# Kernel tuning notes

Hardware: AMD Instinct MI355X
Metric: run time of the kernel (lower is better)

Reference implementation:

```python
import math
import jax, jax.numpy as jnp
import numpy as np

RATIO = 0.1

def setup_inputs() -> dict:
    key = jax.random.key(0)
    ks = jax.random.split(key, 8)
    B, S, D = 8, 4096, 2048
    transformer_out = jax.random.normal(ks[0], (B, S, D), jnp.float32)
    hidden_states = jax.random.normal(ks[1], (B, S, D), jnp.float32)
    lengths = jax.random.randint(ks[2], (B,), S // 2, S + 1)
    attention_mask = (jnp.arange(S)[None, :] < lengths[:, None]).astype(jnp.int32)
    s = 1.0 / math.sqrt(D)
    W1 = jax.random.normal(ks[3], (D, D), jnp.float32) * s
    b1 = jnp.zeros((D,), jnp.float32)
    w2 = jax.random.normal(ks[4], (D,), jnp.float32) * s
    b2 = jnp.zeros((), jnp.float32)
    Wv = jax.random.normal(ks[5], (D, D), jnp.float32) * s
    bv = jnp.zeros((D,), jnp.float32)
    return dict(transformer_out=transformer_out, hidden_states=hidden_states,
                attention_mask=attention_mask, W1=W1, b1=b1, w2=w2, b2=b2, Wv=Wv, bv=bv)

def reference(transformer_out, hidden_states, attention_mask, W1, b1, w2, b2, Wv, bv):
    B, S, D = transformer_out.shape
    M = math.ceil(S * RATIO)  # static upper bound on max_nugget (n_nugget <= ceil(S*ratio))
    # scorer MLP: Linear(D,D) -> ReLU -> Linear(D,1), squeezed
    h = jax.nn.relu(jnp.einsum('bsd,de->bse', transformer_out, W1) + b1)
    scores = jnp.einsum('bse,e->bs', h, w2) + b2                      # [B,S]
    maskb = attention_mask.astype(bool)
    scores = jnp.where(maskb, scores, jnp.finfo(scores.dtype).min)    # masked fill
    n_token = maskb.sum(axis=1)                                        # [B]
    n_nugget = jnp.ceil(n_token.astype(scores.dtype) * RATIO).astype(jnp.int32)
    n_nugget = jnp.minimum(jnp.maximum(n_nugget, 1), n_token)
    nugget_mask = jnp.arange(M)[None, :] < n_nugget[:, None]          # [B,M] ragged validity
    # descending top-k by double argsort, then stable reorder to original token order
    sorted_idx = jnp.argsort(-scores, axis=1)[:, :M]                   # [B,M]
    big = jnp.iinfo(sorted_idx.dtype).max
    resort = jnp.where(nugget_mask, sorted_idx, big)
    indices = jnp.take_along_axis(sorted_idx, jnp.argsort(resort, axis=1), axis=1)
    enc = jnp.take_along_axis(hidden_states, indices[:, :, None], axis=1)  # [B,M,D]
    enc = jnp.einsum('bmd,de->bme', enc, Wv) + bv                      # value_ffn
    nugget_scores = jnp.take_along_axis(scores, indices, axis=1)       # [B,M]
    return enc, nugget_mask, nugget_scores, indices, scores
```

## Files before the change

### kernel.cpp

```cpp
#include <hip/hip_runtime.h>
#include <float.h>
#include <math.h>

typedef _Float16 h16;
typedef _Float16 h16x8 __attribute__((ext_vector_type(8)));
typedef float    f32x4 __attribute__((ext_vector_type(4)));

#define MFMA16(a, b, c) __builtin_amdgcn_mfma_f32_16x16x32_f16((a), (b), (c), 0, 0, 0)

#define B_    8
#define S_    4096
#define D_    2048
#define M_    410
#define MROWS (B_ * S_)
#define R2    (B_ * M_)

#define MASK_FILL (-3.3895313892515355e38f)

#define ENC_OFF  0
#define MASK_OFF (B_ * M_ * D_)
#define NSC_OFF  (MASK_OFF + B_ * M_)
#define IDX_OFF  (NSC_OFF + B_ * M_)
#define SC_OFF   (IDX_OFF + B_ * M_)

#define WS_W1T  ((size_t)0)
#define WS_WVT  ((size_t)8  << 20)
#define WS_PART ((size_t)16 << 20)
#define WS_IDX  ((size_t)17 << 20)
#define WS_NEEDED (((size_t)17 << 20) + R2 * sizeof(int))

__device__ inline float finite_or(float v, float alt) {
    return (v == v && v <= FLT_MAX && v >= -FLT_MAX) ? v : alt;
}

__device__ inline void gload_lds16(const h16* g, h16* l) {
    __builtin_amdgcn_global_load_lds(
        (const __attribute__((address_space(1))) void*)g,
        (__attribute__((address_space(3))) void*)l, 16, 0, 0);
}

__device__ inline h16x8 cvt8(f32x4 a, f32x4 b) {
    h16x8 r;
#pragma unroll
    for (int i = 0; i < 4; ++i) { r[i] = (h16)a[i]; r[i + 4] = (h16)b[i]; }
    return r;
}

__global__ __launch_bounds__(256) void transpose_kernel(
    const float* __restrict__ W1, const float* __restrict__ Wv,
    h16* __restrict__ w1t, h16* __restrict__ wvt)
{
    __shared__ float tile[32][33];
    const float* src = blockIdx.z ? Wv : W1;
    h16* dt = blockIdx.z ? wvt : w1t;
    const int tx = threadIdx.x, ty = threadIdx.y;
    const int n0 = blockIdx.x * 32, k0 = blockIdx.y * 32;
#pragma unroll
    for (int i = 0; i < 4; ++i) {
        int k = k0 + ty + i * 8;
        tile[ty + i * 8][tx] = src[(size_t)k * D_ + n0 + tx];
    }
    __syncthreads();
#pragma unroll
    for (int i = 0; i < 4; ++i) {
        int n = n0 + ty + i * 8;
        dt[(size_t)n * D_ + k0 + tx] = (h16)tile[tx][ty + i * 8];
    }
}

template <int MODE>
__global__ __launch_bounds__(512, 4) void gemm_kernel(
    const float* __restrict__ A,
    const h16* __restrict__ Bt,
    const float* __restrict__ bias,
    const float* __restrict__ w2,
    float* __restrict__ outp,
    const int* __restrict__ gidx)
{
    constexpr int BM = 128, BN = 256, BK = 32;
    constexpr int NT = D_ / BK;
    __shared__ h16 As[3][BM][32];
    __shared__ h16 Bs[3][BN][32];
    __shared__ float red[4][128];

    int pn, pm;
    if constexpr (MODE == 0) {
        pn = blockIdx.y & 7;
        pm = blockIdx.x + 8 * (blockIdx.y >> 3);
    } else {
        pn = blockIdx.x; pm = blockIdx.y;
    }
    const int t = threadIdx.x;
    const int lane = t & 63, wid = t >> 6;
    const int wm = wid >> 2, wn = wid & 3;
    const int l15 = lane & 15, kseg = lane >> 4;
    const int pcf = (kseg ^ ((l15 >> 1) & 3)) * 8;

    const int arow = t >> 2, aseg = t & 3;
    const int pcA = (aseg ^ ((arow >> 1) & 3)) * 8;

    const int lrow   = lane >> 2;
    const int lchunk = (lane & 3) ^ ((lane >> 3) & 3);

    const float* Ap;
    if constexpr (MODE == 0) {
        Ap = A + (size_t)(pm * BM + arow) * D_ + aseg * 8;
    } else {
        int r = pm * BM + arow;
        int rr = (r < R2) ? r : R2 - 1;
        int bb = rr / M_;
        int tok = gidx[rr];
        Ap = A + ((size_t)bb * S_ + tok) * D_ + aseg * 8;
    }
    const h16* gB0 = Bt + (size_t)(pn * BN + 32 * wid + lrow)      * D_ + lchunk * 8;
    const h16* gB1 = Bt + (size_t)(pn * BN + 32 * wid + 16 + lrow) * D_ + lchunk * 8;

    f32x4 acc[4][4] = {};

    f32x4 a0 = *(const f32x4*)Ap, a1 = *(const f32x4*)(Ap + 4);
    *(h16x8*)&As[0][arow][pcA] = cvt8(a0, a1);
    gload_lds16(gB0, &Bs[0][32 * wid][0]);
    gload_lds16(gB1, &Bs[0][32 * wid + 16][0]);
    gB0 += BK; gB1 += BK;
    Ap += BK;
    a0 = *(const f32x4*)Ap; a1 = *(const f32x4*)(Ap + 4);
    gload_lds16(gB0, &Bs[1][32 * wid][0]);
    gload_lds16(gB1, &Bs[1][32 * wid + 16][0]);
    gB0 += BK; gB1 += BK;
    asm volatile("s_waitcnt vmcnt(0) lgkmcnt(0)" ::: "memory");
    __builtin_amdgcn_s_barrier();

    for (int kt = 0; kt < NT; ++kt) {
        const int cb = kt % 3;
        if (kt > 0) {
            if (kt + 1 < NT) {
                asm volatile("s_waitcnt vmcnt(4) lgkmcnt(0)" ::: "memory");
            } else {
                asm volatile("s_waitcnt vmcnt(0) lgkmcnt(0)" ::: "memory");
            }
            __builtin_amdgcn_s_barrier();
        }
        if (kt + 1 < NT) {
            *(h16x8*)&As[(kt + 1) % 3][arow][pcA] = cvt8(a0, a1);
            if (kt + 2 < NT) {
                Ap += BK;
                a0 = *(const f32x4*)Ap; a1 = *(const f32x4*)(Ap + 4);
                const int nb = (kt + 2) % 3;
                gload_lds16(gB0, &Bs[nb][32 * wid][0]);
                gload_lds16(gB1, &Bs[nb][32 * wid + 16][0]);
                gB0 += BK; gB1 += BK;
            }
        }
        h16x8 fa[4];
#pragma unroll
        for (int fm = 0; fm < 4; ++fm) {
            int row = wm * 64 + fm * 16 + l15;
            fa[fm] = *(const h16x8*)&As[cb][row][pcf];
        }
#pragma unroll
        for (int fn = 0; fn < 4; ++fn) {
            int row = wn * 64 + fn * 16 + l15;
            h16x8 fb = *(const h16x8*)&Bs[cb][row][pcf];
#pragma unroll
            for (int fm = 0; fm < 4; ++fm)
                acc[fm][fn] = MFMA16(fa[fm], fb, acc[fm][fn]);
        }
    }
    __syncthreads();

    if constexpr (MODE == 0) {
        float vout[4][4] = {};
#pragma unroll
        for (int fn = 0; fn < 4; ++fn) {
            int ng = pn * BN + wn * 64 + fn * 16 + l15;
            float w = w2[ng], bb = bias[ng];
#pragma unroll
            for (int fm = 0; fm < 4; ++fm)
#pragma unroll
                for (int rg = 0; rg < 4; ++rg) {
                    float c = acc[fm][fn][rg] + bb;
                    c = fmaxf(c, 0.0f);
                    vout[fm][rg] += c * w;
                }
        }
#pragma unroll
        for (int off = 1; off < 16; off <<= 1)
#pragma unroll
            for (int fm = 0; fm < 4; ++fm)
#pragma unroll
                for (int rg = 0; rg < 4; ++rg)
                    vout[fm][rg] += __shfl_xor(vout[fm][rg], off);
        if (l15 == 0) {
#pragma unroll
            for (int fm = 0; fm < 4; ++fm)
#pragma unroll
                for (int rg = 0; rg < 4; ++rg)
                    red[wn][wm * 64 + fm * 16 + kseg * 4 + rg] = vout[fm][rg];
        }
        __syncthreads();
        if (t < 128) {
            float s = red[0][t] + red[1][t] + red[2][t] + red[3][t];
            outp[(size_t)pn * MROWS + pm * BM + t] = s;
        }
    } else {
#pragma unroll
        for (int fn = 0; fn < 4; ++fn) {
            int ng = pn * BN + wn * 64 + fn * 16 + l15;
            float bb = bias[ng];
#pragma unroll
            for (int fm = 0; fm < 4; ++fm) {
                int rbase = pm * BM + wm * 64 + fm * 16 + kseg * 4;
#pragma unroll
                for (int rg = 0; rg < 4; ++rg) {
                    int r = rbase + rg;
                    if (r < R2)
                        outp[(size_t)r * D_ + ng] =
                            finite_or(acc[fm][fn][rg] + bb, 0.0f);
                }
            }
        }
    }
}

__global__ __launch_bounds__(256) void score_reduce_kernel(
    const float* __restrict__ part, const float* __restrict__ b2,
    const int* __restrict__ amask, float* __restrict__ outF)
{
    int m = blockIdx.x * 256 + threadIdx.x;
    float v = b2[0];
#pragma unroll
    for (int p = 0; p < 8; ++p) v += part[(size_t)p * MROWS + m];
    v = finite_or(v, 0.0f);
    if (amask[m] == 0) v = MASK_FILL;
    outF[SC_OFF + m] = v;
}

__global__ __launch_bounds__(1024) void topk_kernel(
    const float* __restrict__ scores, const int* __restrict__ amask,
    float* __restrict__ outF, int* __restrict__ idx_ws)
{
    const int b = blockIdx.x, t = threadIdx.x;
    __shared__ float s[S_];
    __shared__ int perm[S_];
    __shared__ int sel[512];
    __shared__ int wsum[16];

    int cnt = 0;
    for (int i = t; i < S_; i += 1024) {
        float v = scores[b * S_ + i];
        s[i] = v; perm[i] = i;
        cnt += amask[b * S_ + i];
    }
#pragma unroll
    for (int off = 1; off < 64; off <<= 1) cnt += __shfl_xor(cnt, off);
    if ((t & 63) == 0) wsum[t >> 6] = cnt;
    __syncthreads();
    int n_token = 0;
#pragma unroll
    for (int w = 0; w < 16; ++w) n_token += wsum[w];
    int nn = (int)ceilf((float)n_token * 0.1f);
    if (nn < 1) nn = 1;
    if (nn > n_token) nn = n_token;

    for (int k = 2; k <= S_; k <<= 1)
        for (int j = k >> 1; j > 0; j >>= 1) {
            __syncthreads();
            for (int i = t; i < S_; i += 1024) {
                int ixj = i ^ j;
                if (ixj > i) {
                    int a = perm[i], c = perm[ixj];
                    bool ok = (s[a] > s[c]) || (s[a] == s[c] && a < c);
                    if (((i & k) == 0) ? !ok : ok) { perm[i] = c; perm[ixj] = a; }
                }
            }
        }
    __syncthreads();
    for (int i = t; i < 512; i += 1024) sel[i] = (i < nn) ? perm[i] : 0x7fffffff;
    for (int k = 2; k <= 512; k <<= 1)
        for (int j = k >> 1; j > 0; j >>= 1) {
            __syncthreads();
            if (t < 512) {
                int i = t, ixj = i ^ j;
                if (ixj > i) {
                    int a = sel[i], c = sel[ixj];
                    if (((i & k) == 0) ? (a > c) : (a < c)) { sel[i] = c; sel[ixj] = a; }
                }
            }
        }
    __syncthreads();
    for (int m = t; m < M_; m += 1024) {
        int idx = (m < nn) ? sel[m] : perm[m];
        outF[MASK_OFF + b * M_ + m] = (m < nn) ? 1.0f : 0.0f;
        outF[NSC_OFF + b * M_ + m]  = s[idx];
        outF[IDX_OFF + b * M_ + m]  = (float)idx;
        idx_ws[b * M_ + m] = idx;
    }
}

extern "C" void kernel_launch(void* const* d_in, const int* in_sizes, int n_in,
                              void* d_out, int out_size, void* d_ws, size_t ws_size,
                              hipStream_t stream)
{
    const float* T  = (const float*)d_in[0];
    const float* H  = (const float*)d_in[1];
    const int*   AM = (const int*)d_in[2];
    const float* W1 = (const float*)d_in[3];
    const float* b1 = (const float*)d_in[4];
    const float* w2 = (const float*)d_in[5];
    const float* b2 = (const float*)d_in[6];
    const float* Wv = (const float*)d_in[7];
    const float* bv = (const float*)d_in[8];
    float* outF = (float*)d_out;
    char* ws = (char*)d_ws;

    if (ws_size < WS_NEEDED) return;

    h16* w1t  = (h16*)(ws + WS_W1T);
    h16* wvt  = (h16*)(ws + WS_WVT);
    float* part = (float*)(ws + WS_PART);
    int* idxw   = (int*)(ws + WS_IDX);

    transpose_kernel<<<dim3(64, 64, 2), dim3(32, 8), 0, stream>>>(
        W1, Wv, w1t, wvt);
    gemm_kernel<0><<<dim3(8, 256), 512, 0, stream>>>(
        T, w1t, b1, w2, part, nullptr);
    score_reduce_kernel<<<dim3(128), 256, 0, stream>>>(part, b2, AM, outF);
    topk_kernel<<<dim3(8), 1024, 0, stream>>>(outF + SC_OFF, AM, outF, idxw);
    gemm_kernel<1><<<dim3(8, 26), 512, 0, stream>>>(
        H, wvt, bv, nullptr, outF + ENC_OFF, idxw);
}
```

Before: 529.9 us.

## Add 256x256 eight-phase pipelined GEMM kernel for the scorer MLP

Replaces the 128x256 tile GEMM for the scorer with a new 256x256 tile, BK=64 kernel. It double-buffers LDS, loads A through registers with fp32-to-fp16 conversion, and loads B directly into LDS. The inner loop is split into four barrier-separated phases that interleave LDS fragment reads, global prefetch and MFMA quads under raised wave priority. The goal is more data reuse per tile and better overlap of memory traffic with MFMA work. In exchange it uses more LDS and registers and runs at lower occupancy (launch bounds 2), with more barriers per iteration.

```diff
diff --git a/kernel.cpp b/kernel.cpp
--- a/kernel.cpp
+++ b/kernel.cpp
@@ -68,14 +68,157 @@
     }
 }
 
-template <int MODE>
-__global__ __launch_bounds__(512, 4) void gemm_kernel(
+#define PH_SYNC do { __builtin_amdgcn_s_barrier(); \
+    asm volatile("s_waitcnt lgkmcnt(0)" ::: "memory"); \
+    __builtin_amdgcn_sched_barrier(0); } while (0)
+#define PH_END  __builtin_amdgcn_s_barrier()
+
+#define QUAD(mb, nb2) do { \
+    __builtin_amdgcn_s_setprio(1); \
+    _Pragma("unroll") for (int i_ = 0; i_ < 4; ++i_) \
+    _Pragma("unroll") for (int jn_ = 0; jn_ < 2; ++jn_) \
+    _Pragma("unroll") for (int ks_ = 0; ks_ < 2; ++ks_) \
+        acc[(mb) + i_][(nb2) + jn_] = \
+            MFMA16(fa[ks_][i_], fb[ks_][jn_], acc[(mb) + i_][(nb2) + jn_]); \
+    __builtin_amdgcn_s_setprio(0); } while (0)
+
+__global__ __launch_bounds__(512, 2) void gemm8_kernel(
     const float* __restrict__ A,
     const h16* __restrict__ Bt,
     const float* __restrict__ bias,
     const float* __restrict__ w2,
-    float* __restrict__ outp,
-    const int* __restrict__ gidx)
+    float* __restrict__ outp)
+{
+    constexpr int NT = 32;
+    __shared__ h16 As[2][256][64];
+    __shared__ h16 Bs[2][256][64];
+    __shared__ float red[4][256];
+
+    const int pn = blockIdx.y & 7;
+    const int pm = blockIdx.x + 8 * (blockIdx.y >> 3);
+    const int t = threadIdx.x;
+    const int lane = t & 63, wid = t >> 6;
+    const int wm = wid >> 2, wn = wid & 3;
+    const int l15 = lane & 15, kseg = lane >> 4;
+    const int pc0 = kseg ^ (l15 & 7);
+
+    const int sc = (t & 7) ^ ((t >> 3) & 7);
+    const float* Ag = A  + (size_t)(pm * 256 + (t >> 3)) * D_ + sc * 8;
+    const h16*   Bg = Bt + (size_t)(pn * 256 + (t >> 3)) * D_ + sc * 8;
+    char* AsB = (char*)&As[0][0][0];
+    char* BsB = (char*)&Bs[0][0][0];
+
+    f32x4 ar[8];
+    f32x4 acc[8][4] = {};
+    h16x8 fa[2][4], fb[2][2];
+
+    auto A_issue = [&](int kt) {
+#pragma unroll
+        for (int j = 0; j < 4; ++j) {
+            const float* p = Ag + (size_t)j * 64 * D_ + kt * 64;
+            ar[2 * j]     = *(const f32x4*)p;
+            ar[2 * j + 1] = *(const f32x4*)(p + 4);
+        }
+    };
+    auto B_issue = [&](int kt, int nb) {
+#pragma unroll
+        for (int j = 0; j < 4; ++j)
+            gload_lds16(Bg + (size_t)j * 64 * D_ + kt * 64,
+                        (h16*)(BsB + nb * 65536 + j * 8192 + wid * 1024));
+    };
+    auto A_write = [&](int nb) {
+#pragma unroll
+        for (int j = 0; j < 4; ++j)
+            *(h16x8*)(AsB + nb * 65536 + j * 8192 + t * 16) =
+                cvt8(ar[2 * j], ar[2 * j + 1]);
+    };
+    auto LDA = [&](int cb, int mb) {
+#pragma unroll
+        for (int i = 0; i < 4; ++i) {
+            const int row = wm * 128 + (mb + i) * 16 + l15;
+#pragma unroll
+            for (int ks = 0; ks < 2; ++ks)
+                fa[ks][i] = *(const h16x8*)&As[cb][row][(pc0 ^ (ks << 2)) * 8];
+        }
+    };
+    auto LDB = [&](int cb, int nb2) {
+#pragma unroll
+        for (int i = 0; i < 2; ++i) {
+            const int row = wn * 64 + (nb2 + i) * 16 + l15;
+#pragma unroll
+            for (int ks = 0; ks < 2; ++ks)
+                fb[ks][i] = *(const h16x8*)&Bs[cb][row][(pc0 ^ (ks << 2)) * 8];
+        }
+    };
+
+    A_issue(0);
+    B_issue(0, 0);
+    A_write(0);
+    asm volatile("s_waitcnt vmcnt(0) lgkmcnt(0)" ::: "memory");
+    __builtin_amdgcn_s_barrier();
+
+    for (int kt = 0; kt < NT; ++kt) {
+        const int cb = kt & 1;
+        const bool more = (kt + 1 < NT);
+        LDA(cb, 0); LDB(cb, 0);
+        if (more) { A_issue(kt + 1); B_issue(kt + 1, cb ^ 1); }
+        PH_SYNC; QUAD(0, 0); PH_END;
+        LDB(cb, 2);
+        PH_SYNC; QUAD(0, 2); PH_END;
+        LDA(cb, 4);
+        PH_SYNC; QUAD(4, 2); PH_END;
+        LDB(cb, 0);
+        if (more) A_write(cb ^ 1);
+        PH_SYNC; QUAD(4, 0);
+        asm volatile("s_waitcnt vmcnt(0) lgkmcnt(0)" ::: "memory");
+        PH_END;
+    }
+    __syncthreads();
+
+    float vout[8][4];
+#pragma unroll
+    for (int fm = 0; fm < 8; ++fm)
+#pragma unroll
+        for (int rg = 0; rg < 4; ++rg) vout[fm][rg] = 0.0f;
+#pragma unroll
+    for (int fn = 0; fn < 4; ++fn) {
+        int ng = pn * 256 + wn * 64 + fn * 16 + l15;
+        float w = w2[ng], bb = bias[ng];
+#pragma unroll
+        for (int fm = 0; fm < 8; ++fm)
+#pragma unroll
+            for (int rg = 0; rg < 4; ++rg) {
+                float c = acc[fm][fn][rg] + bb;
+                c = fmaxf(c, 0.0f);
+                vout[fm][rg] += c * w;
+            }
+    }
+#pragma unroll
+    for (int off = 1; off < 16; off <<= 1)
+#pragma unroll
+        for (int fm = 0; fm < 8; ++fm)
+#pragma unroll
+            for (int rg = 0; rg < 4; ++rg)
+                vout[fm][rg] += __shfl_xor(vout[fm][rg], off);
+    if (l15 == 0) {
+#pragma unroll
+        for (int fm = 0; fm < 8; ++fm)
+#pragma unroll
+            for (int rg = 0; rg < 4; ++rg)
+                red[wn][wm * 128 + fm * 16 + kseg * 4 + rg] = vout[fm][rg];
+    }
+    __syncthreads();
+    if (t < 256) {
+        float s = red[0][t] + red[1][t] + red[2][t] + red[3][t];
+        outp[(size_t)pn * MROWS + pm * 256 + t] = s;
+    }
+}
+
+template <int MODE>
+__global__ __launch_bounds__(512, 4) void gemm_kernel(
+    const float* __restrict__ A, const h16* __restrict__ Bt,
+    const float* __restrict__ bias, const float* __restrict__ w2,
+    float* __restrict__ outp, const int* __restrict__ gidx)
 {
     constexpr int BM = 128, BN = 256, BK = 32;
     constexpr int NT = D_ / BK;
@@ -83,13 +226,7 @@
     __shared__ h16 Bs[3][BN][32];
     __shared__ float red[4][128];
 
-    int pn, pm;
-    if constexpr (MODE == 0) {
-        pn = blockIdx.y & 7;
-        pm = blockIdx.x + 8 * (blockIdx.y >> 3);
-    } else {
-        pn = blockIdx.x; pm = blockIdx.y;
-    }
+    const int pn = blockIdx.x, pm = blockIdx.y;
     const int t = threadIdx.x;
     const int lane = t & 63, wid = t >> 6;
     const int wm = wid >> 2, wn = wid & 3;
@@ -98,7 +235,6 @@
 
     const int arow = t >> 2, aseg = t & 3;
     const int pcA = (aseg ^ ((arow >> 1) & 3)) * 8;
-
     const int lrow   = lane >> 2;
     const int lchunk = (lane & 3) ^ ((lane >> 3) & 3);
 
@@ -169,39 +305,6 @@
     __syncthreads();
 
     if constexpr (MODE == 0) {
-        float vout[4][4] = {};
-#pragma unroll
-        for (int fn = 0; fn < 4; ++fn) {
-            int ng = pn * BN + wn * 64 + fn * 16 + l15;
-            float w = w2[ng], bb = bias[ng];
-#pragma unroll
-            for (int fm = 0; fm < 4; ++fm)
-#pragma unroll
-                for (int rg = 0; rg < 4; ++rg) {
-                    float c = acc[fm][fn][rg] + bb;
-                    c = fmaxf(c, 0.0f);
-                    vout[fm][rg] += c * w;
-                }
-        }
-#pragma unroll
-        for (int off = 1; off < 16; off <<= 1)
-#pragma unroll
-            for (int fm = 0; fm < 4; ++fm)
-#pragma unroll
-                for (int rg = 0; rg < 4; ++rg)
-                    vout[fm][rg] += __shfl_xor(vout[fm][rg], off);
-        if (l15 == 0) {
-#pragma unroll
-            for (int fm = 0; fm < 4; ++fm)
-#pragma unroll
-                for (int rg = 0; rg < 4; ++rg)
-                    red[wn][wm * 64 + fm * 16 + kseg * 4 + rg] = vout[fm][rg];
-        }
-        __syncthreads();
-        if (t < 128) {
-            float s = red[0][t] + red[1][t] + red[2][t] + red[3][t];
-            outp[(size_t)pn * MROWS + pm * BM + t] = s;
-        }
     } else {
 #pragma unroll
         for (int fn = 0; fn < 4; ++fn) {
@@ -322,8 +425,8 @@
 
     transpose_kernel<<<dim3(64, 64, 2), dim3(32, 8), 0, stream>>>(
         W1, Wv, w1t, wvt);
-    gemm_kernel<0><<<dim3(8, 256), 512, 0, stream>>>(
-        T, w1t, b1, w2, part, nullptr);
+    gemm8_kernel<<<dim3(8, 128), 512, 0, stream>>>(
+        T, w1t, b1, w2, part);
     score_reduce_kernel<<<dim3(128), 256, 0, stream>>>(part, b2, AM, outF);
     topk_kernel<<<dim3(8), 1024, 0, stream>>>(outF + SC_OFF, AM, outF, idxw);
     gemm_kernel<1><<<dim3(8, 26), 512, 0, stream>>>(
```

After: 563.6 us. +6.3%, slower.
